# Performance work log

Hardware: AMD Instinct MI355X
Metric: run time of the kernel (lower is better)

The kernel has to match this reference:

```python
import jax, jax.numpy as jnp
import numpy as np
import math

LEVEL_DIMS = [256, 512, 1024, 2048]
B, P, K, D = 8192, 64, 8, 512
EPS = 1e-5  # torch LayerNorm default eps


def _layernorm(x, g, b):
    m = jnp.mean(x, axis=-1, keepdims=True)
    v = jnp.var(x, axis=-1, keepdims=True)
    return (x - m) / jnp.sqrt(v + EPS) * g + b


def _l2norm(x):
    # F.normalize(dim=-1): x / max(||x||_2, 1e-12)
    n = jnp.sqrt(jnp.sum(x * x, axis=-1, keepdims=True))
    return x / jnp.maximum(n, 1e-12)


def setup_inputs() -> dict:
    key = jax.random.key(0)
    ks = iter(jax.random.split(key, 32))
    inp = {}
    for i, dim in enumerate(LEVEL_DIMS):
        inp[f'pooled_{i}'] = jax.random.normal(next(ks), (B, dim), jnp.float32)
        inp[f'proto_{i}'] = jax.random.normal(next(ks), (P, dim), jnp.float32)
        inp[f'ln_g_{i}'] = jnp.ones((2 * dim,), jnp.float32)
        inp[f'ln_b_{i}'] = jnp.zeros((2 * dim,), jnp.float32)
        inp[f'W_{i}'] = jax.random.normal(next(ks), (2 * dim, D), jnp.float32) * (1.0 / math.sqrt(2 * dim))
        inp[f'b_{i}'] = jnp.zeros((D,), jnp.float32)
    inp['text_base'] = jax.random.normal(next(ks), (K, D), jnp.float32)
    inp['logit_scale'] = jnp.ones((1,), jnp.float32)
    return inp


def reference(pooled_0, pooled_1, pooled_2, pooled_3,
              proto_0, proto_1, proto_2, proto_3,
              ln_g_0, ln_g_1, ln_g_2, ln_g_3,
              ln_b_0, ln_b_1, ln_b_2, ln_b_3,
              W_0, W_1, W_2, W_3,
              b_0, b_1, b_2, b_3,
              text_base, logit_scale):
    pooled = [pooled_0, pooled_1, pooled_2, pooled_3]
    proto = [proto_0, proto_1, proto_2, proto_3]
    ln_g = [ln_g_0, ln_g_1, ln_g_2, ln_g_3]
    ln_b = [ln_b_0, ln_b_1, ln_b_2, ln_b_3]
    Ws = [W_0, W_1, W_2, W_3]
    bs = [b_0, b_1, b_2, b_3]

    # text encoder: CLIP embeddings normalized, text_proj=Identity, normalized again (idempotent)
    text_features = _l2norm(text_base)  # [K, D]

    ctxs = []
    for pl, pr, g, bb, W, b in zip(pooled, proto, ln_g, ln_b, Ws, bs):
        proto_ctx = jnp.broadcast_to(jnp.mean(pr, axis=0, keepdims=True), pl.shape)  # [B, C]
        fused = jnp.concatenate([pl, proto_ctx], axis=1)  # [B, 2C]
        h = jax.nn.relu(_layernorm(fused, g, bb) @ W + b)  # [B, D]
        ctxs.append(_l2norm(h))
    image_contexts = jnp.stack(ctxs, axis=1)  # [B, L, D]

    logits = jnp.einsum('kd,bld->bkl', text_features, image_contexts)
    logits = logits / math.sqrt(D)
    logits = logits * jnp.clip(logit_scale, 1e-4, None)
    return jax.nn.softmax(logits, axis=-1)  # [B, K, L]
```

## Files before the change

kernel.cpp:

```cpp
#include <hip/hip_runtime.h>
#include <stdint.h>

typedef __bf16 bf16x8 __attribute__((ext_vector_type(8)));
typedef float f32x4 __attribute__((ext_vector_type(4)));

#define OFF_ABF   0u
#define OFF_GWT   62914560u
#define OFF_LOG   66846720u
#define OFF_STAT  100401152u
#define OFF_TEXT  100663296u
#define OFF_U     100679680u
#define OFF_GG    100687872u
#define OFF_BB    100696064u
#define OFF_SCAL  100704256u
#define WS_TOTAL  100719872u

__host__ __device__ __forceinline__ size_t abf_off(int l) {
  return (size_t)4194304u * (size_t)((1u << l) - 1u);
}
__host__ __device__ __forceinline__ size_t gwt_off(int l) {
  return (size_t)262144u * (size_t)((1u << l) - 1u);
}

__device__ __forceinline__ unsigned short f2bf(float x) {
  return (unsigned short)((__float_as_uint(x) + 0x8000u) >> 16);
}
__device__ __forceinline__ unsigned pack2(float a, float b) {
  return ((__float_as_uint(a) + 0x8000u) >> 16) |
         ((__float_as_uint(b) + 0x8000u) & 0xffff0000u);
}
__device__ __forceinline__ void async_load16(const void* g, void* l) {
  __builtin_amdgcn_global_load_lds((const __attribute__((address_space(1))) void*)g,
                                   (__attribute__((address_space(3))) void*)l,
                                   16, 0, 0);
}

struct PrepArgs {
  const float* pooled[4];
  const float* proto[4];
  const float* W[4];
  const float* g[4];
  const float* beta[4];
  const float* bias[4];
  const float* text;
  const float* lsc;
  char* ws;
};

__device__ __forceinline__ void loadUnit(f32x4 (&buf)[8], const f32x4* base, int lane) {
#pragma unroll
  for (int i = 0; i < 4; ++i) {
    buf[2 * i]     = base[2 * (lane + 64 * i)];
    buf[2 * i + 1] = base[2 * (lane + 64 * i) + 1];
  }
}

template <int R>
__device__ __forceinline__ void procUnit(const f32x4 (&v)[8], char* Dst, float* st,
                                         int rowBase, int lane) {
  float p1[4], p2[4];
#pragma unroll
  for (int i = 0; i < 4; ++i) {
    f32x4 a = v[2 * i], b = v[2 * i + 1];
    float s1 = ((a[0] + a[1]) + (a[2] + a[3])) + ((b[0] + b[1]) + (b[2] + b[3]));
    float s2 = 0.f;
    s2 = fmaf(a[0], a[0], s2); s2 = fmaf(a[1], a[1], s2);
    s2 = fmaf(a[2], a[2], s2); s2 = fmaf(a[3], a[3], s2);
    s2 = fmaf(b[0], b[0], s2); s2 = fmaf(b[1], b[1], s2);
    s2 = fmaf(b[2], b[2], s2); s2 = fmaf(b[3], b[3], s2);
    p1[i] = s1; p2[i] = s2;
    uint4 o = make_uint4(pack2(a[0], a[1]), pack2(a[2], a[3]),
                         pack2(b[0], b[1]), pack2(b[2], b[3]));
    *(uint4*)(Dst + 16 * (size_t)(lane + 64 * i)) = o;
  }
  if constexpr (R == 1) {
    float s1 = (p1[0] + p1[1]) + (p1[2] + p1[3]);
    float s2 = (p2[0] + p2[1]) + (p2[2] + p2[3]);
#pragma unroll
    for (int off = 1; off < 64; off <<= 1) {
      s1 += __shfl_xor(s1, off); s2 += __shfl_xor(s2, off);
    }
    if (lane == 0) {
      st[2 * (size_t)rowBase] = s1; st[2 * (size_t)rowBase + 1] = s2;
    }
  } else if constexpr (R == 2) {
#pragma unroll
    for (int h = 0; h < 2; ++h) {
      float s1 = p1[2 * h] + p1[2 * h + 1], s2 = p2[2 * h] + p2[2 * h + 1];
#pragma unroll
      for (int off = 1; off < 64; off <<= 1) {
        s1 += __shfl_xor(s1, off); s2 += __shfl_xor(s2, off);
      }
      if (lane == 0) {
        st[2 * (size_t)(rowBase + h)] = s1; st[2 * (size_t)(rowBase + h) + 1] = s2;
      }
    }
  } else if constexpr (R == 4) {
#pragma unroll
    for (int i = 0; i < 4; ++i) {
      float s1 = p1[i], s2 = p2[i];
#pragma unroll
      for (int off = 1; off < 64; off <<= 1) {
        s1 += __shfl_xor(s1, off); s2 += __shfl_xor(s2, off);
      }
      if (lane == 0) {
        st[2 * (size_t)(rowBase + i)] = s1; st[2 * (size_t)(rowBase + i) + 1] = s2;
      }
    }
  } else {
#pragma unroll
    for (int i = 0; i < 4; ++i) {
      float s1 = p1[i], s2 = p2[i];
#pragma unroll
      for (int off = 1; off < 32; off <<= 1) {
        s1 += __shfl_xor(s1, off); s2 += __shfl_xor(s2, off);
      }
      if ((lane & 31) == 0) {
        int row = rowBase + 2 * i + (lane >> 5);
        st[2 * (size_t)row] = s1; st[2 * (size_t)row + 1] = s2;
      }
    }
  }
}

__global__ __launch_bounds__(256, 4) void prep(PrepArgs A) {
  __shared__ unsigned short tile[128][66];
  __shared__ float redG[4][128], redB[4][128], redU[4][128];
  __shared__ float gsh[64], bsh[64], psh[64];
  __shared__ float redP[4][64];
  int t = threadIdx.x, bid = blockIdx.x;
  int w = t >> 6, lane = t & 63;

  if (bid >= 481) {
    int u0 = (bid - 481) * 4 + w;
    int l, uL;
    if (u0 < 8192)       { l = 3; uL = u0; }
    else if (u0 < 12288) { l = 2; uL = u0 - 8192; }
    else if (u0 < 14336) { l = 1; uL = u0 - 12288; }
    else                 { l = 0; uL = u0 - 14336; }
    const f32x4* P = (const f32x4*)A.pooled[l] + (size_t)uL * 512;
    char* Dst = A.ws + OFF_ABF + abf_off(l) + (size_t)uL * 4096;
    float* st = (float*)(A.ws + OFF_STAT) + (size_t)l * 8192 * 2;
    f32x4 v[8];
    loadUnit(v, P, lane);
    if (l == 3)      procUnit<1>(v, Dst, st, uL,     lane);
    else if (l == 2) procUnit<2>(v, Dst, st, uL * 2, lane);
    else if (l == 1) procUnit<4>(v, Dst, st, uL * 4, lane);
    else             procUnit<8>(v, Dst, st, uL * 8, lane);
    return;
  }

  if (bid == 480) {
    int row = t >> 5, l32 = t & 31;
    const float* tr = A.text + row * 512 + l32;
    float v[16];
    float s = 0.f;
#pragma unroll
    for (int i = 0; i < 16; ++i) {
      v[i] = tr[32 * i];
      s = fmaf(v[i], v[i], s);
    }
#pragma unroll
    for (int off = 1; off < 32; off <<= 1) s += __shfl_xor(s, off);
    float inv = 1.0f / fmaxf(sqrtf(s), 1e-12f);
    float* tf = (float*)(A.ws + OFF_TEXT) + row * 512 + l32;
#pragma unroll
    for (int i = 0; i < 16; ++i) tf[32 * i] = v[i] * inv;
    return;
  }

  int l, idl;
  if (bid < 256)      { l = 3; idl = bid; }
  else if (bid < 384) { l = 2; idl = bid - 256; }
  else if (bid < 448) { l = 1; idl = bid - 384; }
  else                { l = 0; idl = bid - 448; }
  int C = 256 << l;
  int sid = idl >> 2, dchunk = idl & 3;
  int j0 = sid * 64, d0 = dchunk * 128;
  bool top = (j0 < C);
  int L = lane;
  float* scal = (float*)(A.ws + OFF_SCAL);

  if (t < 64) {
    gsh[t] = A.g[l][j0 + t];
    bsh[t] = A.beta[l][j0 + t];
  }
  if (!top) {
    const float* pr = A.proto[l];
    int cb0 = j0 - C;
    float s = 0.f;
#pragma unroll
    for (int r = 0; r < 16; ++r) s += pr[(size_t)(w * 16 + r) * C + cb0 + L];
    redP[w][L] = s;
  }
  __syncthreads();
  if (!top) {
    if (t < 64) {
      float pmv = (redP[0][t] + redP[1][t] + redP[2][t] + redP[3][t]) * (1.0f / 64.0f);
      psh[t] = pmv * gsh[t];
      if (dchunk == 0) {
        float s1 = pmv, s2 = pmv * pmv;
#pragma unroll
        for (int off = 1; off < 64; off <<= 1) {
          s1 += __shfl_xor(s1, off);
          s2 += __shfl_xor(s2, off);
        }
        if (t == 0) {
          atomicAdd(&scal[l], s1);
          atomicAdd(&scal[4 + l], s2);
        }
      }
    }
    __syncthreads();
  }

  const float* W = A.W[l];
  float2 v[16];
#pragma unroll
  for (int r = 0; r < 16; ++r) {
    int j = j0 + w * 16 + r;
    v[r] = *(const float2*)(W + (size_t)j * 512 + d0 + 2 * L);
  }
  float gp0 = 0.f, gp1 = 0.f, bp0 = 0.f, bp1 = 0.f, up0 = 0.f, up1 = 0.f;
#pragma unroll
  for (int r = 0; r < 16; ++r) {
    int jl = w * 16 + r;
    float g = gsh[jl], b = bsh[jl];
    gp0 = fmaf(g, v[r].x, gp0); gp1 = fmaf(g, v[r].y, gp1);
    bp0 = fmaf(b, v[r].x, bp0); bp1 = fmaf(b, v[r].y, bp1);
    if (top) {
      tile[2 * L][jl] = f2bf(g * v[r].x);
      tile[2 * L + 1][jl] = f2bf(g * v[r].y);
    } else {
      float p = psh[jl];
      up0 = fmaf(p, v[r].x, up0); up1 = fmaf(p, v[r].y, up1);
    }
  }
  redG[w][2 * L] = gp0; redG[w][2 * L + 1] = gp1;
  redB[w][2 * L] = bp0; redB[w][2 * L + 1] = bp1;
  if (!top) { redU[w][2 * L] = up0; redU[w][2 * L + 1] = up1; }
  __syncthreads();

  if (t < 128) {
    int d = l * 512 + d0 + t;
    float G = redG[0][t] + redG[1][t] + redG[2][t] + redG[3][t];
    float B = redB[0][t] + redB[1][t] + redB[2][t] + redB[3][t];
    atomicAdd(&((float*)(A.ws + OFF_GG))[d], G);
    atomicAdd(&((float*)(A.ws + OFF_BB))[d], B);
    if (!top) {
      float U = redU[0][t] + redU[1][t] + redU[2][t] + redU[3][t];
      atomicAdd(&((float*)(A.ws + OFF_U))[d], U);
    }
  }
  if (top) {
    unsigned short* gwT = (unsigned short*)(A.ws + OFF_GWT + gwt_off(l));
    int d = t >> 1, jh = (t & 1) * 32;
    const unsigned* trow = (const unsigned*)&tile[d][jh];
    uint4 q0 = make_uint4(trow[0], trow[1], trow[2], trow[3]);
    uint4 q1 = make_uint4(trow[4], trow[5], trow[6], trow[7]);
    uint4 q2 = make_uint4(trow[8], trow[9], trow[10], trow[11]);
    uint4 q3 = make_uint4(trow[12], trow[13], trow[14], trow[15]);
    uint4* dst = (uint4*)(gwT + (size_t)(d0 + d) * C + j0 + jh);
    dst[0] = q0; dst[1] = q1; dst[2] = q2; dst[3] = q3;
  }
}

struct G2Args {
  char* ws;
  const float* bias[4];
};

__global__ __launch_bounds__(256, 3) void gemm2(G2Args A) {
  __shared__ __align__(16) char lds[23040];
  char* ws = A.ws;
  int t = threadIdx.x;
  int xcd = blockIdx.x & 7;
  int j   = blockIdx.x >> 3;
  int l   = 3 - (j >> 5);
  int jj  = j & 31;
  int rb  = xcd * 8 + (jj >> 2);
  int cb  = jj & 3;
  int C = 256 << l;
  int m0 = rb * 128, n0 = cb * 128;

  float* uArr  = (float*)(lds + 16384);
  float* gArr  = (float*)(lds + 16896);
  float* bArr  = (float*)(lds + 17408);
  float* rowM  = (float*)(lds + 17920);
  float* rowIS = (float*)(lds + 18432);
  float* textL = (float*)(lds + 18944);
  const float* scal = (const float*)(ws + OFF_SCAL);

  if (t < 128) {
    int idx = l * 512 + n0 + t;
    uArr[t] = ((const float*)(ws + OFF_U))[idx];
    gArr[t] = ((const float*)(ws + OFF_GG))[idx];
    bArr[t] = ((const float*)(ws + OFF_BB))[idx] + A.bias[l][n0 + t];
  } else {
    int r = t - 128;
    const float* st = (const float*)(ws + OFF_STAT) + (size_t)(l * 8192 + m0 + r) * 2;
    float s1 = st[0], s2 = st[1];
    float inv2C = 1.0f / (float)(2 * C);
    float mr = (s1 + scal[l]) * inv2C;
    float var = (s2 + scal[4 + l]) * inv2C - mr * mr;
    rowM[r] = mr;
    rowIS[r] = rsqrtf(var + 1e-5f);
  }
  {
    const float* tf = (const float*)(ws + OFF_TEXT);
#pragma unroll
    for (int i = 0; i < 4; ++i) {
      int idx = t + 256 * i;
      textL[idx] = tf[(idx >> 7) * 512 + n0 + (idx & 127)];
    }
  }

  int w = t >> 6, lane = t & 63, quad = lane >> 4, lc = lane & 15;
  const char* Abf = ws + OFF_ABF + abf_off(l);
  const char* Bw  = ws + OFF_GWT + gwt_off(l);
  const char* aP[2]; const char* bP[2];
  char* aD[2]; char* bD[2];
#pragma unroll
  for (int i = 0; i < 2; ++i) {
    int li = i * 256 + t;
    int rr = li >> 2, kq = li & 3;
    int sw = kq ^ ((rr >> 1) & 3);
    aP[i] = Abf + ((size_t)(m0 + rr) * C + sw * 8) * 2;
    bP[i] = Bw  + ((size_t)(n0 + rr) * C + sw * 8) * 2;
    aD[i] = lds + i * 4096 + w * 1024;
    bD[i] = lds + 8192 + i * 4096 + w * 1024;
  }
  int wr = (w >> 1) * 64, wc = (w & 1) * 64;
  int arow = wr + lc, brow = wc + lc;
  const char* aF = lds + arow * 64 + (quad ^ ((arow >> 1) & 3)) * 16;
  const char* bF = lds + 8192 + brow * 64 + (quad ^ ((brow >> 1) & 3)) * 16;

  f32x4 acc[4][4] = {};
  for (int k0 = 0; k0 < C; k0 += 32) {
    async_load16(aP[0], aD[0]); async_load16(aP[1], aD[1]);
    async_load16(bP[0], bD[0]); async_load16(bP[1], bD[1]);
    aP[0] += 64; aP[1] += 64; bP[0] += 64; bP[1] += 64;
    __syncthreads();
    bf16x8 av[4];
#pragma unroll
    for (int rt = 0; rt < 4; ++rt) av[rt] = *(const bf16x8*)(aF + rt * 1024);
#pragma unroll
    for (int ct = 0; ct < 4; ++ct) {
      bf16x8 bv = *(const bf16x8*)(bF + ct * 1024);
#pragma unroll
      for (int rt = 0; rt < 4; ++rt)
        acc[rt][ct] = __builtin_amdgcn_mfma_f32_16x16x32_bf16(av[rt], bv, acc[rt][ct], 0, 0, 0);
    }
    __syncthreads();
  }

  int slot = cb * 2 + (w & 1);
#pragma unroll
  for (int rt = 0; rt < 4; ++rt) {
#pragma unroll
    for (int reg = 0; reg < 4; ++reg) {
      int ml = wr + rt * 16 + quad * 4 + reg;
      float rm = rowM[ml], ris = rowIS[ml];
      float p[9] = {};
#pragma unroll
      for (int ct = 0; ct < 4; ++ct) {
        int nl = wc + ct * 16 + lc;
        float h = fmaf(acc[rt][ct][reg] + uArr[nl] - rm * gArr[nl], ris, bArr[nl]);
        h = fmaxf(h, 0.f);
        p[8] = fmaf(h, h, p[8]);
#pragma unroll
        for (int k = 0; k < 8; ++k)
          p[k] = fmaf(h, textL[k * 128 + nl], p[k]);
      }
#pragma unroll
      for (int off = 1; off < 16; off <<= 1) {
#pragma unroll
        for (int k = 0; k < 9; ++k) p[k] += __shfl_xor(p[k], off);
      }
      if (lc == 0) {
        float* Lg = (float*)(ws + OFF_LOG) +
                    ((((size_t)l * 8192 + m0 + ml) * 8 + slot) << 4);
#pragma unroll
        for (int k = 0; k < 9; ++k) Lg[k] = p[k];
      }
    }
  }
}

__global__ __launch_bounds__(256) void finishK(const char* ws, const float* lsc,
                                               float* out) {
  int t = threadIdx.x;
  int row = blockIdx.x * 32 + (t >> 3), k = t & 7;
  float scale = fmaxf(lsc[0], 1e-4f) * 0.04419417382415922f;
  float x[4];
#pragma unroll
  for (int l = 0; l < 4; ++l) {
    const float* Lg = (const float*)(ws + OFF_LOG) + (((size_t)l * 8192 + row) << 7);
    float dot = 0.f, nsq = 0.f;
#pragma unroll
    for (int s = 0; s < 8; ++s) {
      dot += Lg[s * 16 + k];
      nsq += Lg[s * 16 + 8];
    }
    x[l] = dot * (scale / fmaxf(sqrtf(nsq), 1e-12f));
  }
  float mx = fmaxf(fmaxf(x[0], x[1]), fmaxf(x[2], x[3]));
  float e0 = __expf(x[0] - mx), e1 = __expf(x[1] - mx);
  float e2 = __expf(x[2] - mx), e3 = __expf(x[3] - mx);
  float inv = 1.0f / (e0 + e1 + e2 + e3);
  ((float4*)out)[(size_t)row * 8 + k] = make_float4(e0 * inv, e1 * inv, e2 * inv, e3 * inv);
}

extern "C" void kernel_launch(void* const* d_in, const int* in_sizes, int n_in,
                              void* d_out, int out_size, void* d_ws, size_t ws_size,
                              hipStream_t stream) {
  (void)n_in; (void)out_size;
  if (ws_size < (size_t)WS_TOTAL) return;
  char* ws = (char*)d_ws;
  bool dict = (in_sizes[1] == 64 * 256);
  PrepArgs pa;
  for (int l = 0; l < 4; ++l) {
    if (dict) {
      pa.pooled[l] = (const float*)d_in[6 * l + 0];
      pa.proto[l]  = (const float*)d_in[6 * l + 1];
      pa.g[l]      = (const float*)d_in[6 * l + 2];
      pa.beta[l]   = (const float*)d_in[6 * l + 3];
      pa.W[l]      = (const float*)d_in[6 * l + 4];
      pa.bias[l]   = (const float*)d_in[6 * l + 5];
    } else {
      pa.pooled[l] = (const float*)d_in[l];
      pa.proto[l]  = (const float*)d_in[4 + l];
      pa.g[l]      = (const float*)d_in[8 + l];
      pa.beta[l]   = (const float*)d_in[12 + l];
      pa.W[l]      = (const float*)d_in[16 + l];
      pa.bias[l]   = (const float*)d_in[20 + l];
    }
  }
  pa.text = (const float*)d_in[24];
  pa.lsc = (const float*)d_in[25];
  pa.ws = ws;

  hipMemsetAsync(ws + OFF_U, 0, 3 * 8192 + 256, stream);

  prep<<<4321, 256, 0, stream>>>(pa);

  G2Args g2;
  g2.ws = ws;
  for (int l = 0; l < 4; ++l) g2.bias[l] = pa.bias[l];
  gemm2<<<1024, 256, 0, stream>>>(g2);
  finishK<<<256, 256, 0, stream>>>(ws, pa.lsc, (float*)d_out);
}
```

Baseline: 276.2 us.

## Double GEMM K-step to 64 with wider swizzle and parallelize finish reduction

The gemm2 main loop now stages a 64-wide K slice per iteration, using a 128-byte row with an 8-way XOR swizzle, which halves the number of barrier pairs per tile. LDS use grows to about 39KB per block, which may limit occupancy under the launch bound of 3. The finishK kernel now assigns one wavefront per row and reduces the 8 slots with cross-lane shuffles instead of serial per-thread loops. It launches 8x more blocks to spread the memory reads.

```diff
diff --git a/kernel.cpp b/kernel.cpp
--- a/kernel.cpp
+++ b/kernel.cpp
@@ -271,7 +271,7 @@
 };
 
 __global__ __launch_bounds__(256, 3) void gemm2(G2Args A) {
-  __shared__ __align__(16) char lds[23040];
+  __shared__ __align__(16) char lds[39424];
   char* ws = A.ws;
   int t = threadIdx.x;
   int xcd = blockIdx.x & 7;
@@ -283,12 +283,12 @@
   int C = 256 << l;
   int m0 = rb * 128, n0 = cb * 128;
 
-  float* uArr  = (float*)(lds + 16384);
-  float* gArr  = (float*)(lds + 16896);
-  float* bArr  = (float*)(lds + 17408);
-  float* rowM  = (float*)(lds + 17920);
-  float* rowIS = (float*)(lds + 18432);
-  float* textL = (float*)(lds + 18944);
+  float* uArr  = (float*)(lds + 32768);
+  float* gArr  = (float*)(lds + 33280);
+  float* bArr  = (float*)(lds + 33792);
+  float* rowM  = (float*)(lds + 34304);
+  float* rowIS = (float*)(lds + 34816);
+  float* textL = (float*)(lds + 35328);
   const float* scal = (const float*)(ws + OFF_SCAL);
 
   if (t < 128) {
@@ -318,35 +318,50 @@
   int w = t >> 6, lane = t & 63, quad = lane >> 4, lc = lane & 15;
   const char* Abf = ws + OFF_ABF + abf_off(l);
   const char* Bw  = ws + OFF_GWT + gwt_off(l);
-  const char* aP[2]; const char* bP[2];
-  char* aD[2]; char* bD[2];
-#pragma unroll
-  for (int i = 0; i < 2; ++i) {
+  const char* aP[4]; const char* bP[4];
+  char* aD[4]; char* bD[4];
+#pragma unroll
+  for (int i = 0; i < 4; ++i) {
     int li = i * 256 + t;
-    int rr = li >> 2, kq = li & 3;
-    int sw = kq ^ ((rr >> 1) & 3);
+    int rr = li >> 3, s = li & 7;
+    int sw = s ^ (rr & 7);
     aP[i] = Abf + ((size_t)(m0 + rr) * C + sw * 8) * 2;
     bP[i] = Bw  + ((size_t)(n0 + rr) * C + sw * 8) * 2;
     aD[i] = lds + i * 4096 + w * 1024;
-    bD[i] = lds + 8192 + i * 4096 + w * 1024;
+    bD[i] = lds + 16384 + i * 4096 + w * 1024;
   }
   int wr = (w >> 1) * 64, wc = (w & 1) * 64;
   int arow = wr + lc, brow = wc + lc;
-  const char* aF = lds + arow * 64 + (quad ^ ((arow >> 1) & 3)) * 16;
-  const char* bF = lds + 8192 + brow * 64 + (quad ^ ((brow >> 1) & 3)) * 16;
+  int am = arow & 7, bm = brow & 7;
+  const char* aF0 = lds + arow * 128 + ((quad)     ^ am) * 16;
+  const char* aF1 = lds + arow * 128 + ((quad + 4) ^ am) * 16;
+  const char* bF0 = lds + 16384 + brow * 128 + ((quad)     ^ bm) * 16;
+  const char* bF1 = lds + 16384 + brow * 128 + ((quad + 4) ^ bm) * 16;
 
   f32x4 acc[4][4] = {};
-  for (int k0 = 0; k0 < C; k0 += 32) {
-    async_load16(aP[0], aD[0]); async_load16(aP[1], aD[1]);
-    async_load16(bP[0], bD[0]); async_load16(bP[1], bD[1]);
-    aP[0] += 64; aP[1] += 64; bP[0] += 64; bP[1] += 64;
+  for (int k0 = 0; k0 < C; k0 += 64) {
+#pragma unroll
+    for (int i = 0; i < 4; ++i) {
+      async_load16(aP[i], aD[i]);
+      async_load16(bP[i], bD[i]);
+      aP[i] += 128; bP[i] += 128;
+    }
     __syncthreads();
     bf16x8 av[4];
 #pragma unroll
-    for (int rt = 0; rt < 4; ++rt) av[rt] = *(const bf16x8*)(aF + rt * 1024);
+    for (int rt = 0; rt < 4; ++rt) av[rt] = *(const bf16x8*)(aF0 + rt * 2048);
 #pragma unroll
     for (int ct = 0; ct < 4; ++ct) {
-      bf16x8 bv = *(const bf16x8*)(bF + ct * 1024);
+      bf16x8 bv = *(const bf16x8*)(bF0 + ct * 2048);
+#pragma unroll
+      for (int rt = 0; rt < 4; ++rt)
+        acc[rt][ct] = __builtin_amdgcn_mfma_f32_16x16x32_bf16(av[rt], bv, acc[rt][ct], 0, 0, 0);
+    }
+#pragma unroll
+    for (int rt = 0; rt < 4; ++rt) av[rt] = *(const bf16x8*)(aF1 + rt * 2048);
+#pragma unroll
+    for (int ct = 0; ct < 4; ++ct) {
+      bf16x8 bv = *(const bf16x8*)(bF1 + ct * 2048);
 #pragma unroll
       for (int rt = 0; rt < 4; ++rt)
         acc[rt][ct] = __builtin_amdgcn_mfma_f32_16x16x32_bf16(av[rt], bv, acc[rt][ct], 0, 0, 0);
@@ -389,26 +404,30 @@
 
 __global__ __launch_bounds__(256) void finishK(const char* ws, const float* lsc,
                                                float* out) {
-  int t = threadIdx.x;
-  int row = blockIdx.x * 32 + (t >> 3), k = t & 7;
+  int t = threadIdx.x, wv = t >> 6, lane = t & 63;
+  int row = blockIdx.x * 4 + wv;
+  int s = lane >> 3, k = lane & 7;
   float scale = fmaxf(lsc[0], 1e-4f) * 0.04419417382415922f;
   float x[4];
 #pragma unroll
   for (int l = 0; l < 4; ++l) {
     const float* Lg = (const float*)(ws + OFF_LOG) + (((size_t)l * 8192 + row) << 7);
-    float dot = 0.f, nsq = 0.f;
-#pragma unroll
-    for (int s = 0; s < 8; ++s) {
-      dot += Lg[s * 16 + k];
-      nsq += Lg[s * 16 + 8];
-    }
-    x[l] = dot * (scale / fmaxf(sqrtf(nsq), 1e-12f));
-  }
-  float mx = fmaxf(fmaxf(x[0], x[1]), fmaxf(x[2], x[3]));
-  float e0 = __expf(x[0] - mx), e1 = __expf(x[1] - mx);
-  float e2 = __expf(x[2] - mx), e3 = __expf(x[3] - mx);
-  float inv = 1.0f / (e0 + e1 + e2 + e3);
-  ((float4*)out)[(size_t)row * 8 + k] = make_float4(e0 * inv, e1 * inv, e2 * inv, e3 * inv);
+    float d = Lg[s * 16 + k];
+    float n = Lg[s * 16 + 8];
+#pragma unroll
+    for (int off = 8; off < 64; off <<= 1) {
+      d += __shfl_xor(d, off);
+      n += __shfl_xor(n, off);
+    }
+    x[l] = d * (scale / fmaxf(sqrtf(n), 1e-12f));
+  }
+  if (s == 0) {
+    float mx = fmaxf(fmaxf(x[0], x[1]), fmaxf(x[2], x[3]));
+    float e0 = __expf(x[0] - mx), e1 = __expf(x[1] - mx);
+    float e2 = __expf(x[2] - mx), e3 = __expf(x[3] - mx);
+    float inv = 1.0f / (e0 + e1 + e2 + e3);
+    ((float4*)out)[(size_t)row * 8 + k] = make_float4(e0 * inv, e1 * inv, e2 * inv, e3 * inv);
+  }
 }
 
 extern "C" void kernel_launch(void* const* d_in, const int* in_sizes, int n_in,
@@ -448,5 +467,5 @@
   g2.ws = ws;
   for (int l = 0; l < 4; ++l) g2.bias[l] = pa.bias[l];
   gemm2<<<1024, 256, 0, stream>>>(g2);
-  finishK<<<256, 256, 0, stream>>>(ws, pa.lsc, (float*)d_out);
-}
+  finishK<<<2048, 256, 0, stream>>>(ws, pa.lsc, (float*)d_out);
+}
```

After: 279.6 us. Within noise of the previous version (+1.2%).
